# Kernel optimization log

Measured on AMD Instinct MI355X. Metric: run time of the kernel, lower is better.

## Reference

```python
import jax, jax.numpy as jnp
import numpy as np


def setup_inputs() -> dict:
    key = jax.random.key(0)
    k1, k2 = jax.random.split(key)
    NUM_INS, NUM_CLASS = 8192, 5000
    # probabilities strictly inside (0,1) so log terms are finite
    output = jax.random.uniform(k1, (NUM_INS, NUM_CLASS), dtype=jnp.float32,
                                minval=1e-6, maxval=1.0 - 1e-6)
    # labels in {0,1,2}; 2 == ignore
    target = jax.random.randint(k2, (NUM_INS, NUM_CLASS), 0, 3, dtype=jnp.int64)
    return {"output": output, "target": target}


def reference(output, target):
    is_pos = target == 1
    is_neg = target == 0
    # masked BCE: -log(p) for positives, -log(1-p) for negatives, 0 where target==2
    per_elem = jnp.where(is_pos, -jnp.log(output),
                         jnp.where(is_neg, -jnp.log1p(-output), 0.0))
    count = jnp.sum(is_pos | is_neg)
    cost = jnp.sum(per_elem) / count.astype(per_elem.dtype)
    return cost
```

## Files before the change

### kernel.cpp

```cpp
#include <hip/hip_runtime.h>


#define GRID_BLOCKS 2000
#define BLOCK 256

typedef __attribute__((ext_vector_type(4))) float f32x4;
typedef __attribute__((ext_vector_type(4))) int   i32x4;

__global__ __launch_bounds__(BLOCK) void bce_reduce_kernel(
    const float* __restrict__ prob,
    const int* __restrict__ tgt,
    float* __restrict__ part_sum,
    unsigned int* __restrict__ part_cnt,
    int n)
{
    const int tid = blockIdx.x * BLOCK + threadIdx.x;
    const int S   = GRID_BLOCKS * BLOCK;
    const int n4  = n >> 2;

    const f32x4* __restrict__ p4 = (const f32x4*)prob;
    const i32x4* __restrict__ t4 = (const i32x4*)tgt;

    float        lsum = 0.0f;
    unsigned int lcnt = 0u;

    #define ACC(P, T)                                   \
    {                                                   \
        float v = ((T) == 1) ? (P) : 1.0f - (P);        \
        bool  c = (unsigned)(T) <= 1u;                  \
        float l = -__logf(v);                           \
        lsum += c ? l : 0.0f;                           \
        lcnt += c ? 1u : 0u;                            \
    }
    #define ACC4(P, T) ACC((P).x,(T).x) ACC((P).y,(T).y) ACC((P).z,(T).z) ACC((P).w,(T).w)

    const int iters = n4 / S;

    int k = iters - 1;
    for (; k >= 1; k -= 2) {
        f32x4 pa = __builtin_nontemporal_load(p4 + (tid + k * S));
        i32x4 ta = __builtin_nontemporal_load(t4 + (tid + k * S));
        f32x4 pb = __builtin_nontemporal_load(p4 + (tid + (k - 1) * S));
        i32x4 tb = __builtin_nontemporal_load(t4 + (tid + (k - 1) * S));
        ACC4(pa, ta)
        ACC4(pb, tb)
    }
    if (k == 0) {
        f32x4 p = __builtin_nontemporal_load(p4 + tid);
        i32x4 t = __builtin_nontemporal_load(t4 + tid);
        ACC4(p, t)
    }

    for (int i = tid + iters * S; i < n4; i += S) {
        f32x4 p = __builtin_nontemporal_load(p4 + i);
        i32x4 t = __builtin_nontemporal_load(t4 + i);
        ACC4(p, t)
    }

    for (int j = (n4 << 2) + tid; j < n; j += S) {
        float p = prob[j];
        int   t = tgt[j];
        ACC(p, t)
    }

    #pragma unroll
    for (int off = 32; off > 0; off >>= 1) {
        lsum += __shfl_down(lsum, off, 64);
        lcnt += __shfl_down(lcnt, off, 64);
    }

    __shared__ float        s_sum[4];
    __shared__ unsigned int s_cnt[4];
    const int lane = threadIdx.x & 63;
    const int wave = threadIdx.x >> 6;
    if (lane == 0) { s_sum[wave] = lsum; s_cnt[wave] = lcnt; }
    __syncthreads();
    if (threadIdx.x == 0) {
        part_sum[blockIdx.x] = s_sum[0] + s_sum[1] + s_sum[2] + s_sum[3];
        part_cnt[blockIdx.x] = s_cnt[0] + s_cnt[1] + s_cnt[2] + s_cnt[3];
    }
}

__global__ __launch_bounds__(BLOCK) void bce_finalize_kernel(
    const float* __restrict__ part_sum,
    const unsigned int* __restrict__ part_cnt,
    float* __restrict__ out)
{
    float        lsum = 0.0f;
    unsigned int lcnt = 0u;
    for (int i = threadIdx.x; i < GRID_BLOCKS; i += BLOCK) {
        lsum += part_sum[i];
        lcnt += part_cnt[i];
    }
    #pragma unroll
    for (int off = 32; off > 0; off >>= 1) {
        lsum += __shfl_down(lsum, off, 64);
        lcnt += __shfl_down(lcnt, off, 64);
    }
    __shared__ float        s_sum[4];
    __shared__ unsigned int s_cnt[4];
    const int lane = threadIdx.x & 63;
    const int wave = threadIdx.x >> 6;
    if (lane == 0) { s_sum[wave] = lsum; s_cnt[wave] = lcnt; }
    __syncthreads();
    if (threadIdx.x == 0) {
        float        bsum = s_sum[0] + s_sum[1] + s_sum[2] + s_sum[3];
        unsigned int bcnt = s_cnt[0] + s_cnt[1] + s_cnt[2] + s_cnt[3];
        out[0] = bsum / (float)bcnt;
    }
}

extern "C" void kernel_launch(void* const* d_in, const int* in_sizes, int n_in,
                              void* d_out, int out_size, void* d_ws, size_t ws_size,
                              hipStream_t stream) {
    const float* prob = (const float*)d_in[0];
    const int*   tgt  = (const int*)d_in[1];
    float*       out  = (float*)d_out;

    const int n = in_sizes[0];

    float*        part_sum = (float*)d_ws;
    unsigned int* part_cnt = (unsigned int*)((char*)d_ws + GRID_BLOCKS * sizeof(float));

    bce_reduce_kernel<<<GRID_BLOCKS, BLOCK, 0, stream>>>(prob, tgt, part_sum, part_cnt, n);
    bce_finalize_kernel<<<1, BLOCK, 0, stream>>>(part_sum, part_cnt, out);
}
```

Baseline: 305.2 us.

## Pack targets into 2-bit codes in a pre-pass before reduction

Adds a pre-pass kernel that reads the int32 target array and packs four 2-bit labels per byte into workspace. The reduce kernel then reads the packed bytes instead of the full target vectors. The intent is to cut target bandwidth in the reduction, but the pre-pass still reads all targets, so total traffic and launch count go up.

```diff
diff --git a/kernel.cpp b/kernel.cpp
--- a/kernel.cpp
+++ b/kernel.cpp
@@ -7,9 +7,39 @@
 typedef __attribute__((ext_vector_type(4))) float f32x4;
 typedef __attribute__((ext_vector_type(4))) int   i32x4;
 
+__global__ __launch_bounds__(BLOCK) void bce_pack_kernel(
+    const int* __restrict__ tgt,
+    unsigned char* __restrict__ packed,
+    int n4)
+{
+    const int tid = blockIdx.x * BLOCK + threadIdx.x;
+    const int S   = GRID_BLOCKS * BLOCK;
+    const i32x4* __restrict__ t4 = (const i32x4*)tgt;
+
+    const int iters = n4 / S;
+    int k = iters - 1;
+    for (; k >= 1; k -= 2) {
+        const int ia = tid + k * S;
+        const int ib = tid + (k - 1) * S;
+        i32x4 a = __builtin_nontemporal_load(t4 + ia);
+        i32x4 b = __builtin_nontemporal_load(t4 + ib);
+        packed[ia] = (unsigned char)(a.x | (a.y << 2) | (a.z << 4) | (a.w << 6));
+        packed[ib] = (unsigned char)(b.x | (b.y << 2) | (b.z << 4) | (b.w << 6));
+    }
+    if (k == 0) {
+        i32x4 a = __builtin_nontemporal_load(t4 + tid);
+        packed[tid] = (unsigned char)(a.x | (a.y << 2) | (a.z << 4) | (a.w << 6));
+    }
+    for (int i = tid + iters * S; i < n4; i += S) {
+        i32x4 a = __builtin_nontemporal_load(t4 + i);
+        packed[i] = (unsigned char)(a.x | (a.y << 2) | (a.z << 4) | (a.w << 6));
+    }
+}
+
 __global__ __launch_bounds__(BLOCK) void bce_reduce_kernel(
     const float* __restrict__ prob,
     const int* __restrict__ tgt,
+    const unsigned char* __restrict__ packed,
     float* __restrict__ part_sum,
     unsigned int* __restrict__ part_cnt,
     int n)
@@ -19,7 +49,6 @@
     const int n4  = n >> 2;
 
     const f32x4* __restrict__ p4 = (const f32x4*)prob;
-    const i32x4* __restrict__ t4 = (const i32x4*)tgt;
 
     float        lsum = 0.0f;
     unsigned int lcnt = 0u;
@@ -32,31 +61,36 @@
         lsum += c ? l : 0.0f;                           \
         lcnt += c ? 1u : 0u;                            \
     }
-    #define ACC4(P, T) ACC((P).x,(T).x) ACC((P).y,(T).y) ACC((P).z,(T).z) ACC((P).w,(T).w)
+    #define ACCB(P, B)                    \
+    {                                     \
+        ACC((P).x, ((B) & 3))             \
+        ACC((P).y, (((B) >> 2) & 3))      \
+        ACC((P).z, (((B) >> 4) & 3))      \
+        ACC((P).w, (((B) >> 6) & 3))      \
+    }
 
     const int iters = n4 / S;
-
     int k = iters - 1;
     for (; k >= 1; k -= 2) {
-        f32x4 pa = __builtin_nontemporal_load(p4 + (tid + k * S));
-        i32x4 ta = __builtin_nontemporal_load(t4 + (tid + k * S));
-        f32x4 pb = __builtin_nontemporal_load(p4 + (tid + (k - 1) * S));
-        i32x4 tb = __builtin_nontemporal_load(t4 + (tid + (k - 1) * S));
-        ACC4(pa, ta)
-        ACC4(pb, tb)
+        const int ia = tid + k * S;
+        const int ib = tid + (k - 1) * S;
+        f32x4 pa = __builtin_nontemporal_load(p4 + ia);
+        f32x4 pb = __builtin_nontemporal_load(p4 + ib);
+        int   ba = packed[ia];
+        int   bb = packed[ib];
+        ACCB(pa, ba)
+        ACCB(pb, bb)
     }
     if (k == 0) {
         f32x4 p = __builtin_nontemporal_load(p4 + tid);
-        i32x4 t = __builtin_nontemporal_load(t4 + tid);
-        ACC4(p, t)
+        int   b = packed[tid];
+        ACCB(p, b)
     }
-
     for (int i = tid + iters * S; i < n4; i += S) {
         f32x4 p = __builtin_nontemporal_load(p4 + i);
-        i32x4 t = __builtin_nontemporal_load(t4 + i);
-        ACC4(p, t)
+        int   b = packed[i];
+        ACCB(p, b)
     }
-
     for (int j = (n4 << 2) + tid; j < n; j += S) {
         float p = prob[j];
         int   t = tgt[j];
@@ -117,11 +151,14 @@
     const int*   tgt  = (const int*)d_in[1];
     float*       out  = (float*)d_out;
 
-    const int n = in_sizes[0];
+    const int n  = in_sizes[0];
+    const int n4 = n >> 2;
 
-    float*        part_sum = (float*)d_ws;
-    unsigned int* part_cnt = (unsigned int*)((char*)d_ws + GRID_BLOCKS * sizeof(float));
+    unsigned char* packed   = (unsigned char*)d_ws;
+    float*         part_sum = (float*)((char*)d_ws + ((size_t)n4 + 255 & ~(size_t)255));
+    unsigned int*  part_cnt = (unsigned int*)((char*)part_sum + GRID_BLOCKS * sizeof(float));
 
-    bce_reduce_kernel<<<GRID_BLOCKS, BLOCK, 0, stream>>>(prob, tgt, part_sum, part_cnt, n);
+    bce_pack_kernel<<<GRID_BLOCKS, BLOCK, 0, stream>>>(tgt, packed, n4);
+    bce_reduce_kernel<<<GRID_BLOCKS, BLOCK, 0, stream>>>(prob, tgt, packed, part_sum, part_cnt, n);
     bce_finalize_kernel<<<1, BLOCK, 0, stream>>>(part_sum, part_cnt, out);
 }
```

Result: slower. 315.9 us (+3.5%).
